# Kernel tuning notes

Hardware: AMD Instinct MI355X
Metric: run time of the kernel (lower is better)

## Reference

```python
import jax, jax.numpy as jnp
import numpy as np

B, C, W, H = 4, 256, 64, 64
DK = 32


def setup_inputs() -> dict:
    key = jax.random.key(0)
    ks = jax.random.split(key, 5)
    x = jax.random.normal(ks[0], (B, C, W, H), dtype=jnp.float32)
    # 1x1 conv weights ~ linear projections; scale like conv default init
    s = 1.0 / np.sqrt(C)
    Wq = jax.random.normal(ks[1], (DK, C), dtype=jnp.float32) * s
    Wk = jax.random.normal(ks[2], (DK, C), dtype=jnp.float32) * s
    Wv = jax.random.normal(ks[3], (C, C), dtype=jnp.float32) * s
    bq = jnp.zeros((DK,), jnp.float32)
    bk = jnp.zeros((DK,), jnp.float32)
    bv = jnp.zeros((C,), jnp.float32)
    # NOTE: module initializes gamma=0 (output == x, zero grads to Q/K/V);
    # use a nonzero value so the attention path is exercised.
    gamma = jax.random.uniform(ks[4], (1,), dtype=jnp.float32) + 0.5
    return {"x": x, "Wq": Wq, "bq": bq, "Wk": Wk, "bk": bk,
            "Wv": Wv, "bv": bv, "gamma": gamma}


def reference(x, Wq, bq, Wk, bk, Wv, bv, gamma):
    b, c, w, h = x.shape
    n = w * h
    xf = x.reshape(b, c, n)                      # [B, C, N]
    q = jnp.einsum('kc,bcn->bkn', Wq, xf) + bq[None, :, None]  # [B, dk, N]
    k = jnp.einsum('kc,bcn->bkn', Wk, xf) + bk[None, :, None]  # [B, dk, N]
    v = jnp.einsum('oc,bcn->bon', Wv, xf) + bv[None, :, None]  # [B, C, N]
    energy = jnp.einsum('bkn,bkm->bnm', q, k)    # [B, N, N] (no 1/sqrt(dk) scale)
    attn = jax.nn.softmax(energy, axis=-1)       # softmax over keys m
    # out[b,c,n] = sum_m v[b,c,m] * attn[b,n,m]  (bmm(V, A^T))
    out = jnp.einsum('bcm,bnm->bcn', v, attn)
    out = out.reshape(b, c, w, h)
    out = gamma[0] * out + x                      # channel_in == channel_out
    return out
```

## Files before the change

### kernel.cpp

```cpp
#include <hip/hip_runtime.h>
#include <hip/hip_bf16.h>
#include <stdint.h>

typedef float f32x16 __attribute__((ext_vector_type(16)));
typedef short bf16x8 __attribute__((ext_vector_type(8)));

#define L2E 1.4426950408889634f
#define ROWPAT(r, hi) (((r) & 3) + 8 * ((r) >> 2) + 4 * (hi))

#define WCATB_OFF 0u
#define QBUF_OFF  163840u
#define KBUF_OFF  1212416u
#define VBUF_OFF  2260992u

static __device__ __forceinline__ ushort f2bf(float f) {
    union { float f; uint32_t u; } v; v.f = f;
    uint32_t u = v.u;
    return (ushort)((u + 0x7fffu + ((u >> 16) & 1u)) >> 16);
}

static __device__ __forceinline__ uint32_t cvtpk(float lo, float hi) {
    uint32_t r;
    asm volatile("v_cvt_pk_bf16_f32 %0, %1, %2" : "=v"(r) : "v"(lo), "v"(hi));
    return r;
}
static __device__ __forceinline__ bf16x8 packP(float p0, float p1, float p2, float p3,
                                               float p4, float p5, float p6, float p7) {
    uint32_t a0 = cvtpk(p0, p1), a1 = cvtpk(p2, p3);
    uint32_t b0 = cvtpk(p4, p5), b1 = cvtpk(p6, p7);
    auto s0 = __builtin_amdgcn_permlane32_swap(a0, b0, false, false);
    auto s1 = __builtin_amdgcn_permlane32_swap(a1, b1, false, false);
    union { uint32_t u[4]; bf16x8 v; } pk;
    pk.u[0] = s0[0];
    pk.u[1] = s1[0];
    pk.u[2] = s0[1];
    pk.u[3] = s1[1];
    return pk.v;
}

__global__ void prep_kernel(const float* __restrict__ Wq, const float* __restrict__ Wk,
                            const float* __restrict__ Wv, ushort* __restrict__ Wcb) {
    int row = blockIdx.x, c = threadIdx.x;
    float v;
    if (row < 32)      v = Wq[row * 256 + c];
    else if (row < 64) v = Wk[(row - 32) * 256 + c];
    else               v = Wv[(row - 64) * 256 + c];
    Wcb[row * 256 + c] = f2bf(v);
}

__global__ __launch_bounds__(256)
void fproj_kernel(const float* __restrict__ x, const ushort* __restrict__ Wcb,
                  const float* __restrict__ bq, const float* __restrict__ bk,
                  const float* __restrict__ bv,
                  ushort* __restrict__ qbuf, ushort* __restrict__ kbuf,
                  ushort* __restrict__ vbuf) {
    __shared__ ushort xt[32 * 264];
    const int tid = threadIdx.x;
    const int b = blockIdx.x >> 7;
    const int n0 = (blockIdx.x & 127) << 5;

    const float* xb = x + (((size_t)b) << 20) + n0;
    #pragma unroll
    for (int i = 0; i < 8; ++i) {
        int task = tid + (i << 8);
        int c = task >> 3, seg = task & 7;
        float4 v = *(const float4*)(xb + (size_t)c * 4096 + seg * 4);
        xt[(seg * 4 + 0) * 264 + c] = f2bf(v.x);
        xt[(seg * 4 + 1) * 264 + c] = f2bf(v.y);
        xt[(seg * 4 + 2) * 264 + c] = f2bf(v.z);
        xt[(seg * 4 + 3) * 264 + c] = f2bf(v.w);
    }
    __syncthreads();

    const int w = tid >> 6, l = tid & 63;
    const int l31 = l & 31, hi = l >> 5;

    for (int cc = w; cc < 10; cc += 4) {
        const int wbase = (cc < 2) ? cc * 32 : (cc - 2) * 32 + 64;
        const ushort* wrow = Wcb + (size_t)(wbase + l31) * 256;
        f32x16 acc = (f32x16)0.0f;
        if (cc < 2) {
            #pragma unroll
            for (int kk = 0; kk < 16; ++kk) {
                bf16x8 xf = *(const bf16x8*)&xt[l31 * 264 + kk * 16 + hi * 8];
                bf16x8 wf = *(const bf16x8*)&wrow[kk * 16 + hi * 8];
                acc = __builtin_amdgcn_mfma_f32_32x32x16_bf16(xf, wf, acc, 0, 0, 0);
            }
            const float bias = (cc == 0) ? bq[l31] : bk[l31];
            const float scale = (cc == 0) ? L2E : 1.0f;
            ushort* dst = (cc == 0) ? qbuf : kbuf;
            #pragma unroll
            for (int r = 0; r < 16; ++r) {
                int n = n0 + ROWPAT(r, hi);
                dst[((size_t)((b << 12) + n)) * 32 + l31] = f2bf((acc[r] + bias) * scale);
            }
        } else {
            #pragma unroll
            for (int kk = 0; kk < 16; ++kk) {
                bf16x8 wf = *(const bf16x8*)&wrow[kk * 16 + hi * 8];
                bf16x8 xf = *(const bf16x8*)&xt[l31 * 264 + kk * 16 + hi * 8];
                acc = __builtin_amdgcn_mfma_f32_32x32x16_bf16(wf, xf, acc, 0, 0, 0);
            }
            #pragma unroll
            for (int r = 0; r < 16; ++r) {
                int c = (wbase - 64) + ROWPAT(r, hi);
                vbuf[((size_t)(b * 256 + c)) * 4096 + n0 + l31] = f2bf(acc[r] + bv[c]);
            }
        }
    }
}

#define KSTR 36
#define VSTR 66
__global__ __launch_bounds__(256, 2)
void attn_kernel(const ushort* __restrict__ qbuf, const ushort* __restrict__ kbuf,
                 const ushort* __restrict__ vbuf, const float* __restrict__ x,
                 const float* __restrict__ gammap, float* __restrict__ out) {
    __shared__ ushort klds[2][64 * KSTR];
    __shared__ ushort vlds[2][256 * VSTR];
    __shared__ float  dlds[2][32];

    const int tid = threadIdx.x;
    const int bid = blockIdx.x;
    const int work = (bid & 7) * 64 + (bid >> 3);
    const int b = work >> 7;
    const int qbase = (work & 127) << 5;
    const int w = tid >> 6, l = tid & 63;
    const int l31 = l & 31, hi = l >> 5;
    const int kh = w >> 1, cp = w & 1;

    const ushort* kb = kbuf + ((size_t)b << 12) * 32;
    const ushort* vb = vbuf + ((size_t)b << 8) * 4096;

    const ushort* qrow = qbuf + ((size_t)((b << 12) + qbase + l31)) * 32;
    const bf16x8 qf0 = *(const bf16x8*)&qrow[hi * 8];
    const bf16x8 qf1 = *(const bf16x8*)&qrow[16 + hi * 8];

    f32x16 acc[4];
    #pragma unroll
    for (int ch = 0; ch < 4; ++ch) acc[ch] = (f32x16)0.0f;
    float dsum = 0.f;

    const int vc = tid >> 3, vs = tid & 7;
    const int krow = tid >> 2, kseg = tid & 3;
    const ushort* vsrc = vb + (size_t)vc * 4096 + vs * 8;
    const ushort* ksrc = kb + (size_t)krow * 32 + kseg * 8;
    uint4 vreg[8], kreg;

    #pragma unroll
    for (int i = 0; i < 8; ++i)
        vreg[i] = *(const uint4*)(vsrc + (size_t)i * 32 * 4096);
    kreg = *(const uint4*)ksrc;
    #pragma unroll
    for (int i = 0; i < 8; ++i)
        *(uint4*)&vlds[0][(vc + 32 * i) * VSTR + vs * 8] = vreg[i];
    *(uint4*)&klds[0][krow * KSTR + kseg * 8] = kreg;
    __syncthreads();

    for (int it = 0; it < 64; ++it) {
        const int cur = it & 1;
        if (it < 63) {
            const size_t m0 = (size_t)(it + 1) << 6;
            #pragma unroll
            for (int i = 0; i < 8; ++i)
                vreg[i] = *(const uint4*)(vsrc + (size_t)i * 32 * 4096 + m0);
            kreg = *(const uint4*)(ksrc + (m0 << 5));
        }

        const int krow_a = (kh * 32 + l31) * KSTR;
        bf16x8 kf0 = *(const bf16x8*)&klds[cur][krow_a + hi * 8];
        bf16x8 kf1 = *(const bf16x8*)&klds[cur][krow_a + 16 + hi * 8];
        f32x16 sT = __builtin_amdgcn_mfma_f32_32x32x16_bf16(kf0, qf0, (f32x16)0.0f, 0, 0, 0);
        sT = __builtin_amdgcn_mfma_f32_32x32x16_bf16(kf1, qf1, sT, 0, 0, 0);

        float p[16];
        #pragma unroll
        for (int r = 0; r < 16; ++r) {
            p[r] = exp2f(sT[r]);
            dsum += p[r];
        }
        bf16x8 pf0 = packP(p[0], p[1], p[2], p[3], p[4], p[5], p[6], p[7]);
        bf16x8 pf1 = packP(p[8], p[9], p[10], p[11], p[12], p[13], p[14], p[15]);

        __builtin_amdgcn_s_setprio(1);
        #pragma unroll
        for (int ch = 0; ch < 4; ++ch) {
            const int crow = (cp * 128 + ch * 32 + l31) * VSTR + kh * 32;
            bf16x8 vfa = *(const bf16x8*)&vlds[cur][crow + hi * 8];
            bf16x8 vfb = *(const bf16x8*)&vlds[cur][crow + 16 + hi * 8];
            acc[ch] = __builtin_amdgcn_mfma_f32_32x32x16_bf16(vfa, pf0, acc[ch], 0, 0, 0);
            acc[ch] = __builtin_amdgcn_mfma_f32_32x32x16_bf16(vfb, pf1, acc[ch], 0, 0, 0);
        }
        __builtin_amdgcn_s_setprio(0);

        if (it < 63) {
            const int nb = cur ^ 1;
            #pragma unroll
            for (int i = 0; i < 8; ++i)
                *(uint4*)&vlds[nb][(vc + 32 * i) * VSTR + vs * 8] = vreg[i];
            *(uint4*)&klds[nb][krow * KSTR + kseg * 8] = kreg;
        }
        __syncthreads();
    }

    const float gam = gammap[0];
    float dall = dsum + __shfl_xor(dsum, 32);
    float* scr = (float*)&vlds[0][0];
    if (kh == 1) {
        #pragma unroll
        for (int ch = 0; ch < 4; ++ch)
            #pragma unroll
            for (int r = 0; r < 16; ++r)
                scr[(((cp * 4 + ch) * 16 + r) << 6) + l] = acc[ch][r];
    }
    if (cp == 0 && l < 32) dlds[kh][l31] = dall;
    __syncthreads();
    if (kh == 0) {
        const float denom = dlds[0][l31] + dlds[1][l31];
        const float ginv = gam / denom;
        const float* xb2 = x + (((size_t)b) << 8) * 4096;
        float* ob = out + (((size_t)b) << 8) * 4096;
        const int q = qbase + l31;
        #pragma unroll
        for (int ch = 0; ch < 4; ++ch) {
            #pragma unroll
            for (int r = 0; r < 16; ++r) {
                int c = cp * 128 + ch * 32 + ROWPAT(r, hi);
                float o = acc[ch][r] + scr[(((cp * 4 + ch) * 16 + r) << 6) + l];
                size_t idx = (size_t)c * 4096 + q;
                ob[idx] = o * ginv + xb2[idx];
            }
        }
    }
}

extern "C" void kernel_launch(void* const* d_in, const int* in_sizes, int n_in,
                              void* d_out, int out_size, void* d_ws, size_t ws_size,
                              hipStream_t stream) {
    (void)in_sizes; (void)n_in; (void)out_size; (void)ws_size;
    const float* x     = (const float*)d_in[0];
    const float* Wq    = (const float*)d_in[1];
    const float* bq    = (const float*)d_in[2];
    const float* Wk    = (const float*)d_in[3];
    const float* bk    = (const float*)d_in[4];
    const float* Wv    = (const float*)d_in[5];
    const float* bv    = (const float*)d_in[6];
    const float* gamma = (const float*)d_in[7];
    float* out = (float*)d_out;

    char* ws = (char*)d_ws;
    ushort* Wcb  = (ushort*)(ws + WCATB_OFF);
    ushort* qbuf = (ushort*)(ws + QBUF_OFF);
    ushort* kbuf = (ushort*)(ws + KBUF_OFF);
    ushort* vbuf = (ushort*)(ws + VBUF_OFF);

    prep_kernel<<<320, 256, 0, stream>>>(Wq, Wk, Wv, Wcb);
    fproj_kernel<<<512, 256, 0, stream>>>(x, Wcb, bq, bk, bv, qbuf, kbuf, vbuf);
    attn_kernel<<<512, 256, 0, stream>>>(qbuf, kbuf, vbuf, x, gamma, out);
}
```

Measured before the change: 107.4 us.

## Software-pipeline QK/exp of next tile with PV MFMAs of previous tile

Restructures the attention main loop into a two-stage software pipeline. Each step computes QK scores, exp and P packing for tile k and loads its V fragments into registers, while the PV MFMAs for tile k-1 run from registers loaded earlier. This is meant to overlap the exp/VALU work and the LDS reads with the matrix-core work instead of running them back to back. In exchange it roughly doubles the live P and V register fragments, which raises register pressure and may lower occupancy. It also adds a barrier before the epilogue reuses LDS as scratch.

```diff
diff --git a/kernel.cpp b/kernel.cpp
--- a/kernel.cpp
+++ b/kernel.cpp
@@ -147,65 +147,102 @@
     const ushort* ksrc = kb + (size_t)krow * 32 + kseg * 8;
     uint4 vreg[8], kreg;
 
-    #pragma unroll
-    for (int i = 0; i < 8; ++i)
-        vreg[i] = *(const uint4*)(vsrc + (size_t)i * 32 * 4096);
-    kreg = *(const uint4*)ksrc;
-    #pragma unroll
-    for (int i = 0; i < 8; ++i)
-        *(uint4*)&vlds[0][(vc + 32 * i) * VSTR + vs * 8] = vreg[i];
-    *(uint4*)&klds[0][krow * KSTR + kseg * 8] = kreg;
-    __syncthreads();
-
-    for (int it = 0; it < 64; ++it) {
-        const int cur = it & 1;
-        if (it < 63) {
-            const size_t m0 = (size_t)(it + 1) << 6;
-            #pragma unroll
-            for (int i = 0; i < 8; ++i)
-                vreg[i] = *(const uint4*)(vsrc + (size_t)i * 32 * 4096 + m0);
-            kreg = *(const uint4*)(ksrc + (m0 << 5));
-        }
-
-        const int krow_a = (kh * 32 + l31) * KSTR;
-        bf16x8 kf0 = *(const bf16x8*)&klds[cur][krow_a + hi * 8];
-        bf16x8 kf1 = *(const bf16x8*)&klds[cur][krow_a + 16 + hi * 8];
-        f32x16 sT = __builtin_amdgcn_mfma_f32_32x32x16_bf16(kf0, qf0, (f32x16)0.0f, 0, 0, 0);
-        sT = __builtin_amdgcn_mfma_f32_32x32x16_bf16(kf1, qf1, sT, 0, 0, 0);
-
-        float p[16];
-        #pragma unroll
-        for (int r = 0; r < 16; ++r) {
-            p[r] = exp2f(sT[r]);
-            dsum += p[r];
-        }
-        bf16x8 pf0 = packP(p[0], p[1], p[2], p[3], p[4], p[5], p[6], p[7]);
-        bf16x8 pf1 = packP(p[8], p[9], p[10], p[11], p[12], p[13], p[14], p[15]);
-
-        __builtin_amdgcn_s_setprio(1);
-        #pragma unroll
-        for (int ch = 0; ch < 4; ++ch) {
-            const int crow = (cp * 128 + ch * 32 + l31) * VSTR + kh * 32;
-            bf16x8 vfa = *(const bf16x8*)&vlds[cur][crow + hi * 8];
-            bf16x8 vfb = *(const bf16x8*)&vlds[cur][crow + 16 + hi * 8];
-            acc[ch] = __builtin_amdgcn_mfma_f32_32x32x16_bf16(vfa, pf0, acc[ch], 0, 0, 0);
-            acc[ch] = __builtin_amdgcn_mfma_f32_32x32x16_bf16(vfb, pf1, acc[ch], 0, 0, 0);
-        }
-        __builtin_amdgcn_s_setprio(0);
-
-        if (it < 63) {
-            const int nb = cur ^ 1;
-            #pragma unroll
-            for (int i = 0; i < 8; ++i)
-                *(uint4*)&vlds[nb][(vc + 32 * i) * VSTR + vs * 8] = vreg[i];
-            *(uint4*)&klds[nb][krow * KSTR + kseg * 8] = kreg;
-        }
+    const int krow_a = (kh * 32 + l31) * KSTR;
+
+    bf16x8 pA0, pA1, pB0, pB1;
+    bf16x8 vA0, vA1, vA2, vA3, vA4, vA5, vA6, vA7;
+    bf16x8 vB0, vB1, vB2, vB3, vB4, vB5, vB6, vB7;
+
+#define QK_EXP_LOAD(CUR, PC0, PC1, VC0, VC1, VC2, VC3, VC4, VC5, VC6, VC7)     \
+    {                                                                          \
+        bf16x8 kf0 = *(const bf16x8*)&klds[CUR][krow_a + hi * 8];              \
+        bf16x8 kf1 = *(const bf16x8*)&klds[CUR][krow_a + 16 + hi * 8];         \
+        f32x16 sT = __builtin_amdgcn_mfma_f32_32x32x16_bf16(kf0, qf0,          \
+                                                    (f32x16)0.0f, 0, 0, 0);    \
+        sT = __builtin_amdgcn_mfma_f32_32x32x16_bf16(kf1, qf1, sT, 0, 0, 0);   \
+        float p[16];                                                           \
+        _Pragma("unroll")                                                      \
+        for (int r = 0; r < 16; ++r) { p[r] = exp2f(sT[r]); dsum += p[r]; }    \
+        PC0 = packP(p[0], p[1], p[2], p[3], p[4], p[5], p[6], p[7]);           \
+        PC1 = packP(p[8], p[9], p[10], p[11], p[12], p[13], p[14], p[15]);     \
+        const int cr0 = (cp * 128 + 0 * 32 + l31) * VSTR + kh * 32;            \
+        const int cr1 = (cp * 128 + 1 * 32 + l31) * VSTR + kh * 32;            \
+        const int cr2 = (cp * 128 + 2 * 32 + l31) * VSTR + kh * 32;            \
+        const int cr3 = (cp * 128 + 3 * 32 + l31) * VSTR + kh * 32;            \
+        VC0 = *(const bf16x8*)&vlds[CUR][cr0 + hi * 8];                        \
+        VC1 = *(const bf16x8*)&vlds[CUR][cr0 + 16 + hi * 8];                   \
+        VC2 = *(const bf16x8*)&vlds[CUR][cr1 + hi * 8];                        \
+        VC3 = *(const bf16x8*)&vlds[CUR][cr1 + 16 + hi * 8];                   \
+        VC4 = *(const bf16x8*)&vlds[CUR][cr2 + hi * 8];                        \
+        VC5 = *(const bf16x8*)&vlds[CUR][cr2 + 16 + hi * 8];                   \
+        VC6 = *(const bf16x8*)&vlds[CUR][cr3 + hi * 8];                        \
+        VC7 = *(const bf16x8*)&vlds[CUR][cr3 + 16 + hi * 8];                   \
+    }
+
+#define PV_OTHER(PO0, PO1, VO0, VO1, VO2, VO3, VO4, VO5, VO6, VO7)             \
+    {                                                                          \
+        __builtin_amdgcn_s_setprio(1);                                         \
+        acc[0] = __builtin_amdgcn_mfma_f32_32x32x16_bf16(VO0, PO0, acc[0], 0, 0, 0); \
+        acc[0] = __builtin_amdgcn_mfma_f32_32x32x16_bf16(VO1, PO1, acc[0], 0, 0, 0); \
+        acc[1] = __builtin_amdgcn_mfma_f32_32x32x16_bf16(VO2, PO0, acc[1], 0, 0, 0); \
+        acc[1] = __builtin_amdgcn_mfma_f32_32x32x16_bf16(VO3, PO1, acc[1], 0, 0, 0); \
+        acc[2] = __builtin_amdgcn_mfma_f32_32x32x16_bf16(VO4, PO0, acc[2], 0, 0, 0); \
+        acc[2] = __builtin_amdgcn_mfma_f32_32x32x16_bf16(VO5, PO1, acc[2], 0, 0, 0); \
+        acc[3] = __builtin_amdgcn_mfma_f32_32x32x16_bf16(VO6, PO0, acc[3], 0, 0, 0); \
+        acc[3] = __builtin_amdgcn_mfma_f32_32x32x16_bf16(VO7, PO1, acc[3], 0, 0, 0); \
+        __builtin_amdgcn_s_setprio(0);                                         \
+    }
+
+#define PREFETCH(KNEXT)                                                        \
+    {                                                                          \
+        const size_t m0 = (size_t)(KNEXT) << 6;                                \
+        _Pragma("unroll")                                                      \
+        for (int i = 0; i < 8; ++i)                                            \
+            vreg[i] = *(const uint4*)(vsrc + (size_t)i * 32 * 4096 + m0);      \
+        kreg = *(const uint4*)(ksrc + (m0 << 5));                              \
+    }
+
+#define STAGE_WRITE(DSTBUF)                                                    \
+    {                                                                          \
+        _Pragma("unroll")                                                      \
+        for (int i = 0; i < 8; ++i)                                            \
+            *(uint4*)&vlds[DSTBUF][(vc + 32 * i) * VSTR + vs * 8] = vreg[i];   \
+        *(uint4*)&klds[DSTBUF][krow * KSTR + kseg * 8] = kreg;                 \
+    }
+
+    PREFETCH(0);
+    STAGE_WRITE(0);
+    __syncthreads();
+    PREFETCH(1);
+    QK_EXP_LOAD(0, pA0, pA1, vA0, vA1, vA2, vA3, vA4, vA5, vA6, vA7);
+    STAGE_WRITE(1);
+    __syncthreads();
+
+    for (int k = 1; k < 62; k += 2) {
+        PREFETCH(k + 1);
+        QK_EXP_LOAD(1, pB0, pB1, vB0, vB1, vB2, vB3, vB4, vB5, vB6, vB7);
+        PV_OTHER(pA0, pA1, vA0, vA1, vA2, vA3, vA4, vA5, vA6, vA7);
+        STAGE_WRITE(0);
         __syncthreads();
-    }
+        PREFETCH(k + 2);
+        QK_EXP_LOAD(0, pA0, pA1, vA0, vA1, vA2, vA3, vA4, vA5, vA6, vA7);
+        PV_OTHER(pB0, pB1, vB0, vB1, vB2, vB3, vB4, vB5, vB6, vB7);
+        STAGE_WRITE(1);
+        __syncthreads();
+    }
+    QK_EXP_LOAD(1, pB0, pB1, vB0, vB1, vB2, vB3, vB4, vB5, vB6, vB7);
+    PV_OTHER(pA0, pA1, vA0, vA1, vA2, vA3, vA4, vA5, vA6, vA7);
+    PV_OTHER(pB0, pB1, vB0, vB1, vB2, vB3, vB4, vB5, vB6, vB7);
+
+#undef QK_EXP_LOAD
+#undef PV_OTHER
+#undef PREFETCH
+#undef STAGE_WRITE
 
     const float gam = gammap[0];
     float dall = dsum + __shfl_xor(dsum, 32);
     float* scr = (float*)&vlds[0][0];
+    __syncthreads();
     if (kh == 1) {
         #pragma unroll
         for (int ch = 0; ch < 4; ++ch)
```

Result: no change. 108.2 us (+0.7%).
